# Optimization experiments

Measured on AMD Instinct MI355X. Metric: run time of the kernel, lower is better.

The kernel has to match this reference:

```python
import jax, jax.numpy as jnp
import numpy as np

N, E, IN_DIM, H, D = 50000, 1600000, 128, 8, 16


def setup_inputs() -> dict:
    key = jax.random.key(0)
    ks = jax.random.split(key, 9)
    s = 1.0 / np.sqrt(IN_DIM)
    return {
        "h": jax.random.normal(ks[0], (N, IN_DIM), dtype=jnp.float32),
        "Wq": jax.random.normal(ks[1], (IN_DIM, H * D), dtype=jnp.float32) * s,
        "bq": jax.random.normal(ks[2], (H * D,), dtype=jnp.float32) * 0.01,
        "Wk": jax.random.normal(ks[3], (IN_DIM, H * D), dtype=jnp.float32) * s,
        "bk": jax.random.normal(ks[4], (H * D,), dtype=jnp.float32) * 0.01,
        "Wv": jax.random.normal(ks[5], (IN_DIM, H * D), dtype=jnp.float32) * s,
        "bv": jax.random.normal(ks[6], (H * D,), dtype=jnp.float32) * 0.01,
        "src": jax.random.randint(ks[7], (E,), 0, N, dtype=jnp.int32),
        "dst": jax.random.randint(ks[8], (E,), 0, N, dtype=jnp.int32),
    }


def reference(h, Wq, bq, Wk, bk, Wv, bv, src, dst):
    n = h.shape[0]
    # node-level projections, reshaped to [N, H, D]
    Q = (h @ Wq + bq).reshape(n, H, D)
    K = (h @ Wk + bk).reshape(n, H, D)
    V = (h @ Wv + bv).reshape(n, H, D)
    # per-edge score: dot(K[src], Q[dst]) / sqrt(D), exp-clamped -> [E, H]
    score = jnp.sum(K[src] * Q[dst], axis=-1) / np.sqrt(D)
    score = jnp.exp(jnp.clip(score, -5.0, 5.0))
    # score-weighted messages scattered into destination nodes
    m = V[src] * score[:, :, None]                    # [E, H, D]
    wV = jax.ops.segment_sum(m, dst, num_segments=n)  # [N, H, D]
    z = jax.ops.segment_sum(score, dst, num_segments=n)  # [N, H]
    h_out = wV / (z[:, :, None] + 1e-6)
    return h_out.reshape(n, H * D)
```

## Files before the change

kernel.cpp:

```cpp
#include <hip/hip_runtime.h>
#include <hip/hip_bf16.h>

#define IN_DIM 128
#define HH 8
#define DD 16
#define HD 128
#define SCAN_B 256
#define BCHUNK 4096

#define MT  32
#define KP  136
#define NCH 128

typedef float f32x4 __attribute__((ext_vector_type(4)));
typedef short s16x8 __attribute__((ext_vector_type(8)));

__device__ __forceinline__ int sniff_fp32(const unsigned short* h_raw) {
  int sane = 0;
#pragma unroll
  for (int i = 0; i < 128; i += 2) {
    const unsigned short u = h_raw[i];
    const int expo = (u >> 7) & 0xFF;
    if (expo >= 112 && expo <= 143) sane++;
  }
  return (sane >= 40) ? 0 : 1;
}

__global__ __launch_bounds__(128) void wt_kernel(
    const unsigned short* __restrict__ h_raw,
    const void* __restrict__ Wq, const void* __restrict__ Wk,
    const void* __restrict__ Wv, __hip_bfloat16* __restrict__ Wt,
    int* __restrict__ flag, int* __restrict__ bucket_cur) {
  const int isf = sniff_fp32(h_raw);
  const int n = blockIdx.x;
  const int k = threadIdx.x;
  if (n == 0) {
    if (k == 0) *flag = isf;
    for (int j = k; j < 258; j += 128) bucket_cur[j] = 0;
  }
  const int mat = n >> 7;
  const int col = n & 127;
  const void* W = (mat == 0) ? Wq : (mat == 1) ? Wk : Wv;
  float v;
  if (isf) v = ((const float*)W)[(size_t)k * HD + col];
  else     v = __bfloat162float(((const __hip_bfloat16*)W)[(size_t)k * HD + col]);
  Wt[(size_t)n * KP + k] = __float2bfloat16(v);
}

__global__ __launch_bounds__(256) void bucketize_kernel(
    const int* __restrict__ src, const int* __restrict__ dst,
    int* __restrict__ bucket_cur, unsigned int* __restrict__ ebuf,
    int ecap, int n_edges) {
  __shared__ int lh[256];
  const int tid = threadIdx.x;
  const int e0 = blockIdx.x * BCHUNK;
  const int e1 = (e0 + BCHUNK < n_edges) ? e0 + BCHUNK : n_edges;
  lh[tid] = 0;
  __syncthreads();
  for (int e = e0 + tid; e < e1; e += 256) atomicAdd(&lh[dst[e] >> 8], 1);
  __syncthreads();
  const int cnt_local = lh[tid];
  int base = 0;
  if (cnt_local > 0)
    base = tid * ecap + atomicAdd(&bucket_cur[tid], cnt_local);
  __syncthreads();
  lh[tid] = base;
  __syncthreads();
  for (int e = e0 + tid; e < e1; e += 256) {
    const int d = dst[e];
    const int pos = atomicAdd(&lh[d >> 8], 1);
    ebuf[pos] = ((unsigned int)src[e] << 16) | (unsigned int)d;
  }
}

__global__ __launch_bounds__(256, 4) void proj_kernel(
    const void* __restrict__ h, const __hip_bfloat16* __restrict__ Wt,
    const void* __restrict__ bq, const void* __restrict__ bk,
    const void* __restrict__ bv,
    __hip_bfloat16* __restrict__ Qb, __hip_bfloat16* __restrict__ KVb,
    const int* __restrict__ flag, int n_nodes) {
  __shared__ short As[MT * KP];

  const int tid = threadIdx.x;
  const int node0 = blockIdx.x * MT;
  const int isf = *flag;

#pragma unroll
  for (int j = 0; j < 8; ++j) {
    const int pid = tid + j * 256;
    const int m = pid >> 6;
    const int kk = (pid & 63) * 2;
    const int g = node0 + m;
    unsigned int pack = 0;
    if (g < n_nodes) {
      if (isf) {
        const float2 f2 = *(const float2*)((const float*)h + (size_t)g * HD + kk);
        const __hip_bfloat16 b0 = __float2bfloat16(f2.x);
        const __hip_bfloat16 b1 = __float2bfloat16(f2.y);
        pack = (unsigned int)(*(const unsigned short*)&b0) |
               ((unsigned int)(*(const unsigned short*)&b1) << 16);
      } else {
        pack = *(const unsigned int*)((const __hip_bfloat16*)h +
                                      (size_t)g * HD + kk);
      }
    }
    *(unsigned int*)&As[m * KP + kk] = pack;
  }
  __syncthreads();

  const int wave = tid >> 6;
  const int lane = tid & 63;
  const int l15 = lane & 15;
  const int quad = lane >> 4;
  const int rg = wave & 1;
  const int th = wave >> 1;

  s16x8 afrag[4];
#pragma unroll
  for (int k4 = 0; k4 < 4; ++k4)
    afrag[k4] = *(const s16x8*)&As[(rg * 16 + l15) * KP + k4 * 32 + quad * 8];

  for (int c = 0; c < 3; ++c) {
    const __hip_bfloat16* Wc = Wt + (size_t)c * NCH * KP;

    f32x4 acc[4];
#pragma unroll
    for (int t = 0; t < 4; ++t) acc[t] = (f32x4){0.f, 0.f, 0.f, 0.f};

#pragma unroll
    for (int t = 0; t < 4; ++t) {
      const int tt = th * 4 + t;
#pragma unroll
      for (int k4 = 0; k4 < 4; ++k4) {
        const s16x8 bfrag = *(const s16x8*)(
            Wc + (tt * 16 + l15) * KP + k4 * 32 + quad * 8);
        acc[t] = __builtin_amdgcn_mfma_f32_16x16x32_bf16(afrag[k4], bfrag,
                                                         acc[t], 0, 0, 0);
      }
    }

    const void* bp = (c == 0) ? bq : (c == 1) ? bk : bv;
#pragma unroll
    for (int t = 0; t < 4; ++t) {
      const int ncol = (th * 4 + t) * 16 + l15;
      const float bias = isf ? ((const float*)bp)[ncol]
                             : __bfloat162float(((const __hip_bfloat16*)bp)[ncol]);
#pragma unroll
      for (int r = 0; r < 4; ++r) {
        const int g = node0 + rg * 16 + quad * 4 + r;
        if (g < n_nodes) {
          const float val = acc[t][r] + bias;
          if (c == 0) {
            Qb[(size_t)g * HD + ncol] = __float2bfloat16(val);
          } else if (c == 1) {
            KVb[(size_t)g * 256 + ncol] = __float2bfloat16(val);
          } else {
            KVb[(size_t)g * 256 + 128 + ncol] = __float2bfloat16(val);
          }
        }
      }
    }
  }
}

__global__ __launch_bounds__(1024) void bucket_csr_kernel(
    const unsigned int* __restrict__ ebuf, const int* __restrict__ bucket_cur,
    int* __restrict__ row_ptr, int* __restrict__ edge_src,
    int n_nodes, int nbuck, int ecap, int n_edges) {
  __shared__ int lc[256];
  __shared__ int sh[256];
  const int b = blockIdx.x;
  const int t = threadIdx.x;

  int v = 0;
  if (t < 256) {
    v = (t < nbuck) ? bucket_cur[t] : 0;
    sh[t] = v;
  }
  __syncthreads();
  for (int off = 1; off < 256; off <<= 1) {
    int add = 0;
    if (t < 256 && t >= off) add = sh[t - off];
    __syncthreads();
    if (t < 256) sh[t] += add;
    __syncthreads();
  }
  if (t < 256) lc[t] = sh[t] - v;
  __syncthreads();
  const int lo_out = lc[b];
  const int size_b = bucket_cur[b];
  const int lo_in = b * ecap;
  const int nbase = b << 8;
  __syncthreads();

  if (t < 256) lc[t] = 0;
  __syncthreads();
  for (int i = t; i < size_b; i += 1024)
    atomicAdd(&lc[(ebuf[lo_in + i] & 0xFFFFu) - nbase], 1);
  __syncthreads();

  int v2 = 0;
  if (t < 256) {
    v2 = lc[t];
    sh[t] = v2;
  }
  __syncthreads();
  for (int off = 1; off < 256; off <<= 1) {
    int add = 0;
    if (t < 256 && t >= off) add = sh[t - off];
    __syncthreads();
    if (t < 256) sh[t] += add;
    __syncthreads();
  }
  const int excl = (t < 256) ? (sh[t] - v2) : 0;

  if (t < 256) {
    const int node = nbase + t;
    if (node < n_nodes) row_ptr[node] = lo_out + excl;
    if (b == nbuck - 1 && t == 255) row_ptr[n_nodes] = n_edges;
  }
  __syncthreads();
  if (t < 256) lc[t] = lo_out + excl;
  __syncthreads();
  for (int i = t; i < size_b; i += 1024) {
    const unsigned int pkd = ebuf[lo_in + i];
    const int pos = atomicAdd(&lc[(pkd & 0xFFFFu) - nbase], 1);
    edge_src[pos] = (int)(pkd >> 16);
  }
}

__global__ __launch_bounds__(256) void hist_kernel(
    const int* __restrict__ dst, int* __restrict__ cnt, int n_edges) {
  const int e = blockIdx.x * blockDim.x + threadIdx.x;
  if (e < n_edges) atomicAdd(&cnt[dst[e]], 1);
}

__global__ __launch_bounds__(256) void scatter_kernel(
    const int* __restrict__ src, const int* __restrict__ dst,
    int* __restrict__ cursor, int* __restrict__ edge_src, int n_edges) {
  const int e = blockIdx.x * blockDim.x + threadIdx.x;
  if (e < n_edges) {
    const int pos = atomicAdd(&cursor[dst[e]], 1);
    edge_src[pos] = src[e];
  }
}

__global__ __launch_bounds__(SCAN_B) void scan1_kernel(
    const int* __restrict__ cnt, int* __restrict__ exs,
    int* __restrict__ bsum, int n) {
  __shared__ int sh[SCAN_B];
  const int t = threadIdx.x;
  const int i = blockIdx.x * SCAN_B + t;
  int v = (i < n) ? cnt[i] : 0;
  sh[t] = v;
  __syncthreads();
  for (int off = 1; off < SCAN_B; off <<= 1) {
    int add = (t >= off) ? sh[t - off] : 0;
    __syncthreads();
    sh[t] += add;
    __syncthreads();
  }
  if (i < n) exs[i] = sh[t] - v;
  if (t == SCAN_B - 1) bsum[blockIdx.x] = sh[t];
}

__global__ __launch_bounds__(SCAN_B) void scan2_kernel(int* __restrict__ bsum,
                                                       int nb) {
  __shared__ int sh[SCAN_B];
  const int t = threadIdx.x;
  if (nb <= SCAN_B) {
    int v = (t < nb) ? bsum[t] : 0;
    sh[t] = v;
    __syncthreads();
    for (int off = 1; off < SCAN_B; off <<= 1) {
      int add = (t >= off) ? sh[t - off] : 0;
      __syncthreads();
      sh[t] += add;
      __syncthreads();
    }
    if (t < nb) bsum[t] = sh[t] - v;
  } else if (t == 0) {
    int run = 0;
    for (int b = 0; b < nb; ++b) { int v = bsum[b]; bsum[b] = run; run += v; }
  }
}

__global__ __launch_bounds__(SCAN_B) void scan3_kernel(
    const int* __restrict__ exs, const int* __restrict__ bsum,
    int* __restrict__ row_ptr, int* __restrict__ cursor, int n, int n_edges) {
  const int i = blockIdx.x * SCAN_B + threadIdx.x;
  if (i < n) {
    const int v = exs[i] + bsum[blockIdx.x];
    row_ptr[i] = v;
    cursor[i] = v;
  }
  if (i == 0) row_ptr[n] = n_edges;
}

__global__ __launch_bounds__(128) void gather_kernel(
    const int* __restrict__ row_ptr, const int* __restrict__ edge_src,
    const __hip_bfloat16* __restrict__ Qb, const __hip_bfloat16* __restrict__ KVb,
    void* __restrict__ out, const int* __restrict__ flag, int n_nodes,
    int node0) {
  __shared__ float vred[HD][17];
  __shared__ float zred[16][HH];

  const int d = node0 + blockIdx.x;
  const int tid = threadIdx.x;

  const int eloc = tid >> 3;
  const int hh8  = tid & 7;

  const int start = row_ptr[d];
  const int deg = row_ptr[d + 1] - start;

  float qreg[16];
  {
    const uint4* qp = (const uint4*)(Qb + (size_t)d * HD + hh8 * 16);
    unsigned int qw[8];
    *(uint4*)&qw[0] = qp[0];
    *(uint4*)&qw[4] = qp[1];
#pragma unroll
    for (int i = 0; i < 8; ++i) {
      qreg[2 * i]     = __uint_as_float(qw[i] << 16) * 0.25f;
      qreg[2 * i + 1] = __uint_as_float(qw[i] & 0xFFFF0000u) * 0.25f;
    }
  }

  float acc[16];
#pragma unroll
  for (int j = 0; j < 16; ++j) acc[j] = 0.0f;
  float zacc = 0.0f;

  int s0 = 0, s1 = 0;
  if (eloc < deg) s0 = edge_src[start + eloc];
  if (eloc + 16 < deg) s1 = edge_src[start + eloc + 16];

  for (int ei = eloc; ei < deg; ei += 32) {
    const int sA = s0;
    const bool hasB = (ei + 16 < deg);
    const int sB = hasB ? s1 : sA;

    const int nx = ei + 32;
    if (nx < deg) s0 = edge_src[start + nx];
    if (nx + 16 < deg) s1 = edge_src[start + nx + 16];

    const uint4* pA = (const uint4*)(KVb + (size_t)sA * 256 + hh8 * 16);
    const uint4* pB = (const uint4*)(KVb + (size_t)sB * 256 + hh8 * 16);
    const uint4 kA0 = pA[0], kA1 = pA[1];
    const uint4 vA0 = pA[16], vA1 = pA[17];
    const uint4 kB0 = pB[0], kB1 = pB[1];
    const uint4 vB0 = pB[16], vB1 = pB[17];

    unsigned int kw[8];
    *(uint4*)&kw[0] = kA0;
    *(uint4*)&kw[4] = kA1;
    float dotA = 0.0f;
#pragma unroll
    for (int i = 0; i < 8; ++i) {
      const float klo = __uint_as_float(kw[i] << 16);
      const float khi = __uint_as_float(kw[i] & 0xFFFF0000u);
      dotA = fmaf(qreg[2 * i], klo, dotA);
      dotA = fmaf(qreg[2 * i + 1], khi, dotA);
    }
    *(uint4*)&kw[0] = kB0;
    *(uint4*)&kw[4] = kB1;
    float dotB = 0.0f;
#pragma unroll
    for (int i = 0; i < 8; ++i) {
      const float klo = __uint_as_float(kw[i] << 16);
      const float khi = __uint_as_float(kw[i] & 0xFFFF0000u);
      dotB = fmaf(qreg[2 * i], klo, dotB);
      dotB = fmaf(qreg[2 * i + 1], khi, dotB);
    }
    const float scoreA = __expf(fminf(fmaxf(dotA, -5.0f), 5.0f));
    float scoreB = __expf(fminf(fmaxf(dotB, -5.0f), 5.0f));
    if (!hasB) scoreB = 0.0f;
    zacc += scoreA + scoreB;

    unsigned int vwA[8], vwB[8];
    *(uint4*)&vwA[0] = vA0;
    *(uint4*)&vwA[4] = vA1;
    *(uint4*)&vwB[0] = vB0;
    *(uint4*)&vwB[4] = vB1;
#pragma unroll
    for (int i = 0; i < 8; ++i) {
      const float vAlo = __uint_as_float(vwA[i] << 16);
      const float vAhi = __uint_as_float(vwA[i] & 0xFFFF0000u);
      const float vBlo = __uint_as_float(vwB[i] << 16);
      const float vBhi = __uint_as_float(vwB[i] & 0xFFFF0000u);
      acc[2 * i]     = fmaf(scoreA, vAlo, acc[2 * i]);
      acc[2 * i]     = fmaf(scoreB, vBlo, acc[2 * i]);
      acc[2 * i + 1] = fmaf(scoreA, vAhi, acc[2 * i + 1]);
      acc[2 * i + 1] = fmaf(scoreB, vBhi, acc[2 * i + 1]);
    }
  }

#pragma unroll
  for (int j = 0; j < 16; ++j) vred[hh8 * 16 + j][eloc] = acc[j];
  zred[eloc][hh8] = zacc;
  __syncthreads();

  const int hd16 = tid >> 4;
  float sumV = 0.0f;
#pragma unroll
  for (int i = 0; i < 16; ++i) sumV += vred[tid][i];
  float sumZ = 0.0f;
#pragma unroll
  for (int i = 0; i < 16; ++i) sumZ += zred[i][hd16];

  const float r = sumV / (sumZ + 1e-6f);
  const size_t o = (size_t)d * HD + tid;
  if (*flag) ((float*)out)[o] = r;
  else       ((__hip_bfloat16*)out)[o] = __float2bfloat16(r);
}

extern "C" void kernel_launch(void* const* d_in, const int* in_sizes, int n_in,
                              void* d_out, int out_size, void* d_ws, size_t ws_size,
                              hipStream_t stream) {
  const void* h  = d_in[0];
  const void* Wq = d_in[1];
  const void* bq = d_in[2];
  const void* Wk = d_in[3];
  const void* bk = d_in[4];
  const void* Wv = d_in[5];
  const void* bv = d_in[6];
  const int* src = (const int*)d_in[7];
  const int* dst = (const int*)d_in[8];

  const int n_nodes = in_sizes[0] / IN_DIM;
  const int n_edges = in_sizes[7];
  const int nb = (n_nodes + SCAN_B - 1) / SCAN_B;
  const int nbuck = (n_nodes + 255) >> 8;

  int ecap = ((2 * (n_edges / (nbuck > 0 ? nbuck : 1)) + 255) / 256) * 256;
  if (ecap < 4096) ecap = 4096;

  char* p = (char*)d_ws;
  int* flag = (int*)p;                       p += 256;
  __hip_bfloat16* Qb = (__hip_bfloat16*)p;   p += (size_t)n_nodes * HD * 2;
  __hip_bfloat16* KVb = (__hip_bfloat16*)p;  p += (size_t)n_nodes * 256 * 2;
  __hip_bfloat16* Wt = (__hip_bfloat16*)p;   p += ((size_t)384 * KP * 2 + 255) / 256 * 256;
  int* bucket_cur = (int*)p;                 p += 258 * 4 + 248;
  int* row_ptr = (int*)p;                    p += (size_t)(n_nodes + 1 + 63) / 64 * 64 * 4;
  int* edge_src = (int*)p;                   p += (size_t)n_edges * 4;
  unsigned int* ebuf = (unsigned int*)p;     p += (size_t)nbuck * ecap * 4;
  int* cnt = (int*)p;                        p += (size_t)n_nodes * 4;
  int* exs = (int*)p;                        p += (size_t)n_nodes * 4;
  int* bsum = (int*)p;                       p += (size_t)(nb + 1) * 4;
  int* cursor = (int*)p;                     p += (size_t)n_nodes * 4;

  wt_kernel<<<384, 128, 0, stream>>>((const unsigned short*)h, Wq, Wk, Wv, Wt,
                                     flag, bucket_cur);

  const int pgrid = (n_nodes + MT - 1) / MT;
  const int nchunkB = (n_edges + BCHUNK - 1) / BCHUNK;

  if (n_nodes <= 65536) {
    bucketize_kernel<<<nchunkB, 256, 0, stream>>>(src, dst, bucket_cur,
                                                  ebuf, ecap, n_edges);
    proj_kernel<<<pgrid, 256, 0, stream>>>(h, Wt, bq, bk, bv, Qb, KVb,
                                           flag, n_nodes);
    bucket_csr_kernel<<<nbuck, 1024, 0, stream>>>(ebuf, bucket_cur, row_ptr,
                                                  edge_src, n_nodes, nbuck,
                                                  ecap, n_edges);
  } else {
    proj_kernel<<<pgrid, 256, 0, stream>>>(h, Wt, bq, bk, bv, Qb, KVb,
                                           flag, n_nodes);
    hipMemsetAsync(cnt, 0, (size_t)n_nodes * sizeof(int), stream);
    const int eb = 256;
    const int egrid = (n_edges + eb - 1) / eb;
    hist_kernel<<<egrid, eb, 0, stream>>>(dst, cnt, n_edges);
    scan1_kernel<<<nb, SCAN_B, 0, stream>>>(cnt, exs, bsum, n_nodes);
    scan2_kernel<<<1, SCAN_B, 0, stream>>>(bsum, nb);
    scan3_kernel<<<nb, SCAN_B, 0, stream>>>(exs, bsum, row_ptr, cursor,
                                            n_nodes, n_edges);
    scatter_kernel<<<egrid, eb, 0, stream>>>(src, dst, cursor, edge_src,
                                             n_edges);
  }

  if (n_nodes > 30000) {
    const int s = (n_nodes + 2) / 3;
    const int r2 = n_nodes - 2 * s;
    gather_kernel<<<s, 128, 0, stream>>>(row_ptr, edge_src, Qb, KVb,
                                         d_out, flag, n_nodes, 0);
    gather_kernel<<<s, 128, 0, stream>>>(row_ptr, edge_src, Qb, KVb,
                                         d_out, flag, n_nodes, s);
    gather_kernel<<<r2, 128, 0, stream>>>(row_ptr, edge_src, Qb, KVb,
                                          d_out, flag, n_nodes, 2 * s);
  } else {
    gather_kernel<<<n_nodes, 128, 0, stream>>>(row_ptr, edge_src, Qb, KVb,
                                               d_out, flag, n_nodes, 0);
  }
}
```

Before: 278.0 us.

## Fuse bucket CSR build into projection kernel via block-index dispatch

Merges the per-bucket CSR construction into the projection GEMM kernel. The first nbuck blocks run the CSR build with 256 threads, and the remaining blocks do the projection. This removes one kernel launch and lets the CSR build run concurrently with the projection on idle CUs. In exchange, each CSR block now has 256 threads instead of 1024, so per-bucket work is more serialized. The CSR blocks also reuse the GEMM shared-memory tile and its launch bounds.

```diff
diff --git a/kernel.cpp b/kernel.cpp
--- a/kernel.cpp
+++ b/kernel.cpp
@@ -73,16 +73,74 @@
   }
 }
 
-__global__ __launch_bounds__(256, 4) void proj_kernel(
+__global__ __launch_bounds__(256, 4) void proj_csr_kernel(
     const void* __restrict__ h, const __hip_bfloat16* __restrict__ Wt,
     const void* __restrict__ bq, const void* __restrict__ bk,
     const void* __restrict__ bv,
     __hip_bfloat16* __restrict__ Qb, __hip_bfloat16* __restrict__ KVb,
-    const int* __restrict__ flag, int n_nodes) {
+    const int* __restrict__ flag, int n_nodes,
+    const unsigned int* __restrict__ ebuf, const int* __restrict__ bucket_cur,
+    int* __restrict__ row_ptr, int* __restrict__ edge_src,
+    int nbuck, int ecap, int n_edges, int ncsr) {
   __shared__ short As[MT * KP];
 
   const int tid = threadIdx.x;
-  const int node0 = blockIdx.x * MT;
+
+  if (blockIdx.x < ncsr) {
+    int* lc = (int*)As;
+    int* sh = (int*)As + 256;
+    const int b = blockIdx.x;
+
+    const int v = (tid < nbuck) ? bucket_cur[tid] : 0;
+    sh[tid] = v;
+    __syncthreads();
+    for (int off = 1; off < 256; off <<= 1) {
+      int add = (tid >= off) ? sh[tid - off] : 0;
+      __syncthreads();
+      sh[tid] += add;
+      __syncthreads();
+    }
+    lc[tid] = sh[tid] - v;
+    __syncthreads();
+    const int lo_out = lc[b];
+    const int size_b = bucket_cur[b];
+    const int lo_in = b * ecap;
+    const int nbase = b << 8;
+    __syncthreads();
+
+    lc[tid] = 0;
+    __syncthreads();
+    for (int i = tid; i < size_b; i += 256)
+      atomicAdd(&lc[(ebuf[lo_in + i] & 0xFFFFu) - nbase], 1);
+    __syncthreads();
+
+    const int v2 = lc[tid];
+    sh[tid] = v2;
+    __syncthreads();
+    for (int off = 1; off < 256; off <<= 1) {
+      int add = (tid >= off) ? sh[tid - off] : 0;
+      __syncthreads();
+      sh[tid] += add;
+      __syncthreads();
+    }
+    const int excl = sh[tid] - v2;
+
+    const int node = nbase + tid;
+    if (node < n_nodes) row_ptr[node] = lo_out + excl;
+    if (b == nbuck - 1 && tid == 255) row_ptr[n_nodes] = n_edges;
+
+    __syncthreads();
+    lc[tid] = lo_out + excl;
+    __syncthreads();
+    for (int i = tid; i < size_b; i += 256) {
+      const unsigned int pkd = ebuf[lo_in + i];
+      const int pos = atomicAdd(&lc[(pkd & 0xFFFFu) - nbase], 1);
+      edge_src[pos] = (int)(pkd >> 16);
+    }
+    return;
+  }
+
+  const int node0 = (blockIdx.x - ncsr) * MT;
   const int isf = *flag;
 
 #pragma unroll
@@ -163,72 +221,6 @@
   }
 }
 
-__global__ __launch_bounds__(1024) void bucket_csr_kernel(
-    const unsigned int* __restrict__ ebuf, const int* __restrict__ bucket_cur,
-    int* __restrict__ row_ptr, int* __restrict__ edge_src,
-    int n_nodes, int nbuck, int ecap, int n_edges) {
-  __shared__ int lc[256];
-  __shared__ int sh[256];
-  const int b = blockIdx.x;
-  const int t = threadIdx.x;
-
-  int v = 0;
-  if (t < 256) {
-    v = (t < nbuck) ? bucket_cur[t] : 0;
-    sh[t] = v;
-  }
-  __syncthreads();
-  for (int off = 1; off < 256; off <<= 1) {
-    int add = 0;
-    if (t < 256 && t >= off) add = sh[t - off];
-    __syncthreads();
-    if (t < 256) sh[t] += add;
-    __syncthreads();
-  }
-  if (t < 256) lc[t] = sh[t] - v;
-  __syncthreads();
-  const int lo_out = lc[b];
-  const int size_b = bucket_cur[b];
-  const int lo_in = b * ecap;
-  const int nbase = b << 8;
-  __syncthreads();
-
-  if (t < 256) lc[t] = 0;
-  __syncthreads();
-  for (int i = t; i < size_b; i += 1024)
-    atomicAdd(&lc[(ebuf[lo_in + i] & 0xFFFFu) - nbase], 1);
-  __syncthreads();
-
-  int v2 = 0;
-  if (t < 256) {
-    v2 = lc[t];
-    sh[t] = v2;
-  }
-  __syncthreads();
-  for (int off = 1; off < 256; off <<= 1) {
-    int add = 0;
-    if (t < 256 && t >= off) add = sh[t - off];
-    __syncthreads();
-    if (t < 256) sh[t] += add;
-    __syncthreads();
-  }
-  const int excl = (t < 256) ? (sh[t] - v2) : 0;
-
-  if (t < 256) {
-    const int node = nbase + t;
-    if (node < n_nodes) row_ptr[node] = lo_out + excl;
-    if (b == nbuck - 1 && t == 255) row_ptr[n_nodes] = n_edges;
-  }
-  __syncthreads();
-  if (t < 256) lc[t] = lo_out + excl;
-  __syncthreads();
-  for (int i = t; i < size_b; i += 1024) {
-    const unsigned int pkd = ebuf[lo_in + i];
-    const int pos = atomicAdd(&lc[(pkd & 0xFFFFu) - nbase], 1);
-    edge_src[pos] = (int)(pkd >> 16);
-  }
-}
-
 __global__ __launch_bounds__(256) void hist_kernel(
     const int* __restrict__ dst, int* __restrict__ cnt, int n_edges) {
   const int e = blockIdx.x * blockDim.x + threadIdx.x;
@@ -459,14 +451,13 @@
   if (n_nodes <= 65536) {
     bucketize_kernel<<<nchunkB, 256, 0, stream>>>(src, dst, bucket_cur,
                                                   ebuf, ecap, n_edges);
-    proj_kernel<<<pgrid, 256, 0, stream>>>(h, Wt, bq, bk, bv, Qb, KVb,
-                                           flag, n_nodes);
-    bucket_csr_kernel<<<nbuck, 1024, 0, stream>>>(ebuf, bucket_cur, row_ptr,
-                                                  edge_src, n_nodes, nbuck,
-                                                  ecap, n_edges);
+    proj_csr_kernel<<<nbuck + pgrid, 256, 0, stream>>>(
+        h, Wt, bq, bk, bv, Qb, KVb, flag, n_nodes,
+        ebuf, bucket_cur, row_ptr, edge_src, nbuck, ecap, n_edges, nbuck);
   } else {
-    proj_kernel<<<pgrid, 256, 0, stream>>>(h, Wt, bq, bk, bv, Qb, KVb,
-                                           flag, n_nodes);
+    proj_csr_kernel<<<pgrid, 256, 0, stream>>>(
+        h, Wt, bq, bk, bv, Qb, KVb, flag, n_nodes,
+        ebuf, bucket_cur, row_ptr, edge_src, nbuck, ecap, n_edges, 0);
     hipMemsetAsync(cnt, 0, (size_t)n_nodes * sizeof(int), stream);
     const int eb = 256;
     const int egrid = (n_edges + eb - 1) / eb;
```

Result: no change. 280.6 us (+0.9%).
